# Kernel optimization log

Measured on AMD Instinct MI355X. Metric: run time of the kernel, lower is better.

Reference implementation:

```python
import jax, jax.numpy as jnp
import numpy as np

N_NODES = 50000
N_EDGES = 625000
D = 128


def setup_inputs() -> dict:
    key = jax.random.key(0)
    kx, ks, kr, kw, kb = jax.random.split(key, 5)
    x = jax.random.normal(kx, (N_NODES, D), dtype=jnp.float32)
    senders = jax.random.randint(ks, (N_EDGES,), 0, N_NODES, dtype=jnp.int64)
    receivers = jax.random.randint(kr, (N_EDGES,), 0, N_NODES, dtype=jnp.int64)
    # nn.Linear(2*D, D): weight [D, 2*D], bias [D]
    lim = 1.0 / np.sqrt(2 * D)
    W = jax.random.uniform(kw, (D, 2 * D), minval=-lim, maxval=lim, dtype=jnp.float32)
    b = jax.random.uniform(kb, (D,), minval=-lim, maxval=lim, dtype=jnp.float32)
    return {"x": x, "senders": senders, "receivers": receivers, "n_nodes": N_NODES, "W": W, "b": b}


def reference(x, senders, receivers, n_nodes, W, b):
    # Add self loops (with_self=True)
    self_idx = jnp.arange(n_nodes, dtype=senders.dtype)
    s = jnp.concatenate([senders, self_idx])   # [E + N]
    r = jnp.concatenate([receivers, self_idx]) # [E + N]

    ones = jnp.ones(r.shape[0], dtype=x.dtype)
    # degree_norm=True branch (note: mirrors the original's naming exactly:
    # 'out_degree' counted over receivers, 'in_degree' over senders)
    out_degree = jax.ops.segment_sum(ones, r, num_segments=n_nodes)  # [N]
    in_degree = jax.ops.segment_sum(ones, s, num_segments=n_nodes)   # [N]
    out_degree_norm = jax.lax.rsqrt(jnp.maximum(out_degree, 1.0))
    in_degree_norm = jax.lax.rsqrt(jnp.maximum(in_degree, 1.0))

    # Gather sender embeddings, scale, scatter-add to receivers
    sender_emb = x[s] * out_degree_norm[s][:, None]  # [E+N, D]
    aggregated = jax.ops.segment_sum(sender_emb, r, num_segments=n_nodes)  # [N, D]

    # edge_count over receivers == out_degree (same scatter), clamped
    edge_count = jnp.maximum(out_degree, 1.0)
    aggregated = aggregated / edge_count[:, None]
    aggregated = aggregated * in_degree_norm[:, None]

    combined = jnp.concatenate([x, aggregated], axis=1)  # [N, 2D]
    return combined @ W.T + b
```

## Files before the change

kernel.cpp:

```cpp
#include <hip/hip_runtime.h>

#define DIM 128
#define BM 128
#define BK 32
#define BINSZ 128
#define EPB 2048

typedef __attribute__((ext_vector_type(8))) short short8;
typedef __attribute__((ext_vector_type(4))) float f32x4;

__device__ __forceinline__ unsigned short f2bf(float f) {
    unsigned int b = __float_as_uint(f);
    return (unsigned short)((b + 0x7fffu + ((b >> 16) & 1u)) >> 16);
}
__device__ __forceinline__ float bf_lo(unsigned int u) { return __uint_as_float(u << 16); }
__device__ __forceinline__ float bf_hi(unsigned int u) { return __uint_as_float(u & 0xffff0000u); }
__device__ __forceinline__ unsigned int pack2(float a, float b) {
    return (unsigned int)f2bf(a) | ((unsigned int)f2bf(b) << 16);
}
__device__ __forceinline__ uint2 pack4(float4 v) {
    uint2 r; r.x = pack2(v.x, v.y); r.y = pack2(v.z, v.w); return r;
}

__global__ __launch_bounds__(256) void hist_kernel(
        const int* __restrict__ receivers,
        const float4* __restrict__ W4, uint2* __restrict__ Wb4,
        int* __restrict__ Hr, int* __restrict__ deg_s,
        int E, int nbin, int nw4, int N) {
    __shared__ int hr[512];
    int t = threadIdx.x;

    int gi = blockIdx.x * 256 + t;
    if (gi < nw4) Wb4[gi] = pack4(W4[gi]);
    for (int i = gi; i < N; i += gridDim.x * 256) deg_s[i] = 0;

    for (int b = t; b < nbin; b += 256) hr[b] = 0;
    __syncthreads();
    int base = blockIdx.x * EPB;
    for (int k = 0; k < EPB; k += 256) {
        int e = base + k + t;
        if (e < E) atomicAdd(&hr[receivers[e] >> 7], 1);
    }
    __syncthreads();
    size_t ho = (size_t)blockIdx.x * nbin;
    for (int b = t; b < nbin; b += 256) Hr[ho + b] = hr[b];
}

__global__ __launch_bounds__(512) void scan_bins_kernel(
        int* __restrict__ Hr, int* __restrict__ tot_r, int NAB, int nbin) {
    __shared__ int sr[512];
    int b = blockIdx.x, t = threadIdx.x;
    int vr = (t < NAB) ? Hr[(size_t)t * nbin + b] : 0;
    sr[t] = vr;
    __syncthreads();
    for (int off = 1; off < 512; off <<= 1) {
        int ur = (t >= off) ? sr[t - off] : 0;
        __syncthreads();
        sr[t] += ur;
        __syncthreads();
    }
    if (t < NAB) Hr[(size_t)t * nbin + b] = sr[t] - vr;
    if (t == 511) tot_r[b] = sr[511];
}

__global__ __launch_bounds__(512) void scan_base_kernel(
        const int* __restrict__ tot_r, int* __restrict__ base_r,
        int* __restrict__ row_start, int nbin, int N, int E) {
    __shared__ int sr[512];
    int t = threadIdx.x;
    int vr = (t < nbin) ? tot_r[t] : 0;
    sr[t] = vr;
    __syncthreads();
    for (int off = 1; off < 512; off <<= 1) {
        int ur = (t >= off) ? sr[t - off] : 0;
        __syncthreads();
        sr[t] += ur;
        __syncthreads();
    }
    if (t < nbin) base_r[t] = sr[t] - vr;
    if (t == 0) { base_r[nbin] = E; row_start[N] = E; }
}

__global__ __launch_bounds__(256) void scatter_kernel(
        const int* __restrict__ senders, const int* __restrict__ receivers,
        const int* __restrict__ Hr, const int* __restrict__ base_r,
        unsigned int* __restrict__ bucket_r, int* __restrict__ deg_s,
        int E, int nbin) {
    __shared__ int br_[512];
    int t = threadIdx.x;
    size_t ho = (size_t)blockIdx.x * nbin;
    for (int b = t; b < nbin; b += 256) br_[b] = base_r[b] + Hr[ho + b];
    __syncthreads();
    int base = blockIdx.x * EPB;
    for (int k = 0; k < EPB; k += 256) {
        int e = base + k + t;
        if (e < E) {
            int s = senders[e], r = receivers[e];
            int pr = atomicAdd(&br_[r >> 7], 1);
            bucket_r[pr] = ((unsigned int)(r & 127) << 16) | (unsigned int)s;
            atomicAdd(&deg_s[s], 1);
        }
    }
}

__global__ __launch_bounds__(256) void fine_kernel(
        const unsigned int* __restrict__ bucket_r,
        const int* __restrict__ base_r,
        const int* __restrict__ deg_s,
        const float4* __restrict__ x4,
        uint2* __restrict__ xb2,
        int* __restrict__ edge_src,
        int* __restrict__ row_start,
        float* __restrict__ fs,
        float* __restrict__ sc,
        int N) {
    __shared__ int fine[BINSZ], fstart[BINSZ];
    int b = blockIdx.x, t = threadIdx.x;
    if (t < BINSZ) fine[t] = 0;
    __syncthreads();

    int loR = base_r[b], hiR = base_r[b + 1];
    for (int i = loR + t; i < hiR; i += 256)
        atomicAdd(&fine[bucket_r[i] >> 16], 1);
    __syncthreads();

    if (t < BINSZ) fstart[t] = fine[t];
    __syncthreads();
    for (int off = 1; off < BINSZ; off <<= 1) {
        int u = (t < BINSZ && t >= off) ? fstart[t - off] : 0;
        __syncthreads();
        if (t < BINSZ) fstart[t] += u;
        __syncthreads();
    }
    if (t < BINSZ) {
        int excl = fstart[t] - fine[t];
        int node = b * BINSZ + t;
        if (node < N) {
            float od = (float)(fine[t] + 1);
            row_start[node] = loR + excl;
            sc[node] = rsqrtf(od);
            fs[node] = rsqrtf((float)(deg_s[node] + 1)) / od;
        }
        fstart[t] = excl;
    }
    __syncthreads();

    for (int i = loR + t; i < hiR; i += 256) {
        unsigned int u = bucket_r[i];
        int pos = atomicAdd(&fstart[u >> 16], 1);
        edge_src[loR + pos] = (int)(u & 0xFFFFu);
    }

    int nrow0 = b * BINSZ;
    for (int idx = t; idx < BINSZ * 32; idx += 256) {
        int row = idx >> 5, c = idx & 31;
        int node = nrow0 + row;
        if (node < N) xb2[(size_t)node * 32 + c] = pack4(x4[(size_t)node * 32 + c]);
    }
}

__global__ __launch_bounds__(512) void gemm_kernel(
        const unsigned short* __restrict__ x_bf,
        const int* __restrict__ edge_src,
        const int* __restrict__ row_start,
        const float* __restrict__ fs,
        const float* __restrict__ sc,
        const unsigned short* __restrict__ W_bf,
        const float* __restrict__ bias,
        float* __restrict__ out, int N) {
    __shared__ unsigned short As[BM * BK];
    __shared__ unsigned short Bs[DIM * BK];
    __shared__ unsigned short Agg[BM][136];

    int t    = threadIdx.x;
    int lane = t & 63;
    int w    = t >> 6;
    int wr   = w >> 2, wc = w & 3;
    int row0 = blockIdx.x * BM;
    const uint4* xb4 = (const uint4*)x_bf;

    {
        int grp = lane >> 4;
        int gl  = lane & 15;
        for (int it = 0; it < 4; ++it) {
            int nl = it * 32 + w * 4 + grp;
            int n  = row0 + nl;
            bool valid = (n < N);
            int start = 0, deg = 0;
            if (valid) { start = row_start[n]; deg = row_start[n + 1] - start; }
            int md = deg;
            md = max(md, __shfl_xor(md, 16));
            md = max(md, __shfl_xor(md, 32));

            float a[8];
#pragma unroll
            for (int q = 0; q < 8; q++) a[q] = 0.f;

            for (int base = 0; base < md; base += 16) {
                int e = base + gl;
                int src = -1; float scv = 0.f;
                if (e < deg) { src = edge_src[start + e]; scv = sc[src]; }
#pragma unroll
                for (int j = 0; j < 16; j++) {
                    int   s  = __shfl(src, (grp << 4) | j);
                    float sj = __shfl(scv, (grp << 4) | j);
                    if (s >= 0) {
                        uint4 u = xb4[(size_t)s * 16 + gl];
                        a[0] = fmaf(sj, bf_lo(u.x), a[0]);
                        a[1] = fmaf(sj, bf_hi(u.x), a[1]);
                        a[2] = fmaf(sj, bf_lo(u.y), a[2]);
                        a[3] = fmaf(sj, bf_hi(u.y), a[3]);
                        a[4] = fmaf(sj, bf_lo(u.z), a[4]);
                        a[5] = fmaf(sj, bf_hi(u.z), a[5]);
                        a[6] = fmaf(sj, bf_lo(u.w), a[6]);
                        a[7] = fmaf(sj, bf_hi(u.w), a[7]);
                    }
                }
            }

            uint4 o = make_uint4(0u, 0u, 0u, 0u);
            if (valid) {
                float f = fs[n], scn = sc[n];
                uint4 u = xb4[(size_t)n * 16 + gl];
                a[0] = (a[0] + bf_lo(u.x) * scn) * f;
                a[1] = (a[1] + bf_hi(u.x) * scn) * f;
                a[2] = (a[2] + bf_lo(u.y) * scn) * f;
                a[3] = (a[3] + bf_hi(u.y) * scn) * f;
                a[4] = (a[4] + bf_lo(u.z) * scn) * f;
                a[5] = (a[5] + bf_hi(u.z) * scn) * f;
                a[6] = (a[6] + bf_lo(u.w) * scn) * f;
                a[7] = (a[7] + bf_hi(u.w) * scn) * f;
                o.x = pack2(a[0], a[1]); o.y = pack2(a[2], a[3]);
                o.z = pack2(a[4], a[5]); o.w = pack2(a[6], a[7]);
            }
            *(uint4*)&Agg[nl][gl * 8] = o;
        }
    }
    __syncthreads();

    f32x4 acc[4][2];
#pragma unroll
    for (int i = 0; i < 4; i++)
#pragma unroll
        for (int j = 0; j < 2; j++) acc[i][j] = (f32x4){0.f, 0.f, 0.f, 0.f};

    for (int kt = 0; kt < 8; kt++) {
        int k0 = (kt & 3) * BK;
        if (kt < 4) {
            int row = t >> 2, ch = t & 3;
            uint4 v = *(const uint4*)&x_bf[(size_t)(row0 + row) * 128 + k0 + ch * 8];
            *(uint4*)&As[row * BK + ch * 8] = v;
        }
        {
            int n = t >> 2, ch = t & 3;
            uint4 v = *(const uint4*)&W_bf[(size_t)n * 256 + kt * BK + ch * 8];
            *(uint4*)&Bs[n * BK + ch * 8] = v;
        }
        __syncthreads();

        short8 a[4], b[2];
        if (kt < 4) {
#pragma unroll
            for (int i = 0; i < 4; i++)
                a[i] = *(const short8*)&As[(wr * 64 + i * 16 + (lane & 15)) * BK + (lane >> 4) * 8];
        } else {
#pragma unroll
            for (int i = 0; i < 4; i++)
                a[i] = *(const short8*)&Agg[wr * 64 + i * 16 + (lane & 15)][k0 + (lane >> 4) * 8];
        }
#pragma unroll
        for (int j = 0; j < 2; j++)
            b[j] = *(const short8*)&Bs[(wc * 32 + j * 16 + (lane & 15)) * BK + (lane >> 4) * 8];
#pragma unroll
        for (int i = 0; i < 4; i++)
#pragma unroll
            for (int j = 0; j < 2; j++)
                acc[i][j] = __builtin_amdgcn_mfma_f32_16x16x32_bf16(a[i], b[j], acc[i][j], 0, 0, 0);
        __syncthreads();
    }

    int cq = lane >> 4;
    int cl = lane & 15;
#pragma unroll
    for (int j = 0; j < 2; j++) {
        int col = wc * 32 + j * 16 + cl;
        float bb = bias[col];
#pragma unroll
        for (int i = 0; i < 4; i++) {
            int rbase = row0 + wr * 64 + i * 16 + cq * 4;
#pragma unroll
            for (int r = 0; r < 4; r++) {
                int row = rbase + r;
                if (row < N) out[(size_t)row * DIM + col] = acc[i][j][r] + bb;
            }
        }
    }
}

extern "C" void kernel_launch(void* const* d_in, const int* in_sizes, int n_in,
                              void* d_out, int out_size, void* d_ws, size_t ws_size,
                              hipStream_t stream) {
    const float* x         = (const float*)d_in[0];
    const int*   senders   = (const int*)d_in[1];
    const int*   receivers = (const int*)d_in[2];
    const float* W         = (const float*)d_in[4];
    const float* bias      = (const float*)d_in[5];
    float*       out       = (float*)d_out;

    int N    = in_sizes[0] / DIM;
    int E    = in_sizes[1];
    int nbin = (N + BINSZ - 1) / BINSZ;
    int NAB  = (E + EPB - 1) / EPB;
    int NP   = ((N + BM - 1) / BM) * BM;

    char* ws = (char*)d_ws;
    size_t off = 0;
    #define WS_ALLOC(ptrtype, name, bytes) \
        ptrtype name = (ptrtype)(ws + off); off += (((size_t)(bytes)) + 255) & ~(size_t)255;
    WS_ALLOC(int*,            tot_r,     (size_t)nbin * 4)
    WS_ALLOC(int*,            base_r,    (size_t)(nbin + 1) * 4)
    WS_ALLOC(int*,            row_start, (size_t)(N + 1) * 4)
    WS_ALLOC(float*,          fs,        (size_t)N * 4)
    WS_ALLOC(float*,          sc,        (size_t)N * 4)
    WS_ALLOC(int*,            deg_s,     (size_t)N * 4)
    WS_ALLOC(int*,            edge_src,  (size_t)E * 4)
    WS_ALLOC(unsigned short*, x_bf,      (size_t)NP * DIM * 2)
    WS_ALLOC(unsigned short*, W_bf,      (size_t)DIM * 256 * 2)
    WS_ALLOC(unsigned int*,   bucket_r,  (size_t)E * 4)
    WS_ALLOC(int*,            Hr,        (size_t)NAB * nbin * 4)
    #undef WS_ALLOC

    int nw4 = DIM * 256 / 4;

    hist_kernel<<<NAB, 256, 0, stream>>>(receivers,
                                         (const float4*)W, (uint2*)W_bf,
                                         Hr, deg_s, E, nbin, nw4, N);
    scan_bins_kernel<<<nbin, 512, 0, stream>>>(Hr, tot_r, NAB, nbin);
    scan_base_kernel<<<1, 512, 0, stream>>>(tot_r, base_r, row_start, nbin, N, E);
    scatter_kernel<<<NAB, 256, 0, stream>>>(senders, receivers, Hr, base_r,
                                            bucket_r, deg_s, E, nbin);
    fine_kernel<<<nbin, 256, 0, stream>>>(bucket_r, base_r, deg_s,
                                          (const float4*)x, (uint2*)x_bf,
                                          edge_src, row_start, fs, sc, N);
    gemm_kernel<<<(N + BM - 1) / BM, 512, 0, stream>>>(
        x_bf, edge_src, row_start, fs, sc, W_bf, bias, out, N);
}
```

Baseline: 196.3 us.

## Split neighbor gather into its own kernel and pack source index with bf16 scale

Moves the per-node neighbor aggregation out of the GEMM kernel into a separate gather kernel with one 16-lane group per node across many small blocks. The result goes to a bf16 buffer in global memory that the GEMM then streams through shared memory like x. The sender index and its bf16-rounded scale are packed into one 32-bit word, so each edge needs one shuffle instead of two. This aims to improve occupancy and load balance of the latency-bound gather, at the cost of an extra launch, a global round trip for the aggregate, and rounding the scale to bf16.

```diff
diff --git a/kernel.cpp b/kernel.cpp
--- a/kernel.cpp
+++ b/kernel.cpp
@@ -138,7 +138,7 @@
         if (node < N) {
             float od = (float)(fine[t] + 1);
             row_start[node] = loR + excl;
-            sc[node] = rsqrtf(od);
+            sc[node] = __uint_as_float((unsigned int)f2bf(rsqrtf(od)) << 16);
             fs[node] = rsqrtf((float)(deg_s[node] + 1)) / od;
         }
         fstart[t] = excl;
@@ -159,84 +159,89 @@
     }
 }
 
-__global__ __launch_bounds__(512) void gemm_kernel(
-        const unsigned short* __restrict__ x_bf,
+__global__ __launch_bounds__(256) void gather_kernel(
+        const uint4* __restrict__ xb4,
         const int* __restrict__ edge_src,
         const int* __restrict__ row_start,
         const float* __restrict__ fs,
         const float* __restrict__ sc,
+        uint4* __restrict__ aggb4,
+        int N) {
+    int lane = threadIdx.x & 63;
+    int grp  = lane >> 4;
+    int gl   = lane & 15;
+    int wid  = (blockIdx.x * blockDim.x + threadIdx.x) >> 6;
+    int n    = wid * 4 + grp;
+    bool valid = (n < N);
+
+    int start = 0, deg = 0;
+    if (valid) { start = row_start[n]; deg = row_start[n + 1] - start; }
+    int md = deg;
+    md = max(md, __shfl_xor(md, 16));
+    md = max(md, __shfl_xor(md, 32));
+
+    float a[8];
+#pragma unroll
+    for (int q = 0; q < 8; q++) a[q] = 0.f;
+
+    for (int base = 0; base < md; base += 16) {
+        int e = base + gl;
+        unsigned int pk = 0xFFFFFFFFu;
+        if (e < deg) {
+            int s = edge_src[start + e];
+            pk = (unsigned int)s | (__float_as_uint(sc[s]) & 0xffff0000u);
+        }
+#pragma unroll
+        for (int j = 0; j < 16; j++) {
+            unsigned int u = (unsigned int)__shfl((int)pk, (grp << 4) | j);
+            if (u != 0xFFFFFFFFu) {
+                int   s  = (int)(u & 0xFFFFu);
+                float sj = bf_hi(u);
+                uint4 v  = xb4[(size_t)s * 16 + gl];
+                a[0] = fmaf(sj, bf_lo(v.x), a[0]);
+                a[1] = fmaf(sj, bf_hi(v.x), a[1]);
+                a[2] = fmaf(sj, bf_lo(v.y), a[2]);
+                a[3] = fmaf(sj, bf_hi(v.y), a[3]);
+                a[4] = fmaf(sj, bf_lo(v.z), a[4]);
+                a[5] = fmaf(sj, bf_hi(v.z), a[5]);
+                a[6] = fmaf(sj, bf_lo(v.w), a[6]);
+                a[7] = fmaf(sj, bf_hi(v.w), a[7]);
+            }
+        }
+    }
+
+    if (valid) {
+        float f = fs[n], scn = sc[n];
+        uint4 u = xb4[(size_t)n * 16 + gl];
+        a[0] = (a[0] + bf_lo(u.x) * scn) * f;
+        a[1] = (a[1] + bf_hi(u.x) * scn) * f;
+        a[2] = (a[2] + bf_lo(u.y) * scn) * f;
+        a[3] = (a[3] + bf_hi(u.y) * scn) * f;
+        a[4] = (a[4] + bf_lo(u.z) * scn) * f;
+        a[5] = (a[5] + bf_hi(u.z) * scn) * f;
+        a[6] = (a[6] + bf_lo(u.w) * scn) * f;
+        a[7] = (a[7] + bf_hi(u.w) * scn) * f;
+        uint4 o;
+        o.x = pack2(a[0], a[1]); o.y = pack2(a[2], a[3]);
+        o.z = pack2(a[4], a[5]); o.w = pack2(a[6], a[7]);
+        aggb4[(size_t)n * 16 + gl] = o;
+    }
+}
+
+__global__ __launch_bounds__(512) void gemm_kernel(
+        const unsigned short* __restrict__ x_bf,
+        const unsigned short* __restrict__ agg_bf,
         const unsigned short* __restrict__ W_bf,
         const float* __restrict__ bias,
         float* __restrict__ out, int N) {
     __shared__ unsigned short As[BM * BK];
     __shared__ unsigned short Bs[DIM * BK];
-    __shared__ unsigned short Agg[BM][136];
 
     int t    = threadIdx.x;
     int lane = t & 63;
     int w    = t >> 6;
     int wr   = w >> 2, wc = w & 3;
     int row0 = blockIdx.x * BM;
-    const uint4* xb4 = (const uint4*)x_bf;
-
-    {
-        int grp = lane >> 4;
-        int gl  = lane & 15;
-        for (int it = 0; it < 4; ++it) {
-            int nl = it * 32 + w * 4 + grp;
-            int n  = row0 + nl;
-            bool valid = (n < N);
-            int start = 0, deg = 0;
-            if (valid) { start = row_start[n]; deg = row_start[n + 1] - start; }
-            int md = deg;
-            md = max(md, __shfl_xor(md, 16));
-            md = max(md, __shfl_xor(md, 32));
-
-            float a[8];
-#pragma unroll
-            for (int q = 0; q < 8; q++) a[q] = 0.f;
-
-            for (int base = 0; base < md; base += 16) {
-                int e = base + gl;
-                int src = -1; float scv = 0.f;
-                if (e < deg) { src = edge_src[start + e]; scv = sc[src]; }
-#pragma unroll
-                for (int j = 0; j < 16; j++) {
-                    int   s  = __shfl(src, (grp << 4) | j);
-                    float sj = __shfl(scv, (grp << 4) | j);
-                    if (s >= 0) {
-                        uint4 u = xb4[(size_t)s * 16 + gl];
-                        a[0] = fmaf(sj, bf_lo(u.x), a[0]);
-                        a[1] = fmaf(sj, bf_hi(u.x), a[1]);
-                        a[2] = fmaf(sj, bf_lo(u.y), a[2]);
-                        a[3] = fmaf(sj, bf_hi(u.y), a[3]);
-                        a[4] = fmaf(sj, bf_lo(u.z), a[4]);
-                        a[5] = fmaf(sj, bf_hi(u.z), a[5]);
-                        a[6] = fmaf(sj, bf_lo(u.w), a[6]);
-                        a[7] = fmaf(sj, bf_hi(u.w), a[7]);
-                    }
-                }
-            }
-
-            uint4 o = make_uint4(0u, 0u, 0u, 0u);
-            if (valid) {
-                float f = fs[n], scn = sc[n];
-                uint4 u = xb4[(size_t)n * 16 + gl];
-                a[0] = (a[0] + bf_lo(u.x) * scn) * f;
-                a[1] = (a[1] + bf_hi(u.x) * scn) * f;
-                a[2] = (a[2] + bf_lo(u.y) * scn) * f;
-                a[3] = (a[3] + bf_hi(u.y) * scn) * f;
-                a[4] = (a[4] + bf_lo(u.z) * scn) * f;
-                a[5] = (a[5] + bf_hi(u.z) * scn) * f;
-                a[6] = (a[6] + bf_lo(u.w) * scn) * f;
-                a[7] = (a[7] + bf_hi(u.w) * scn) * f;
-                o.x = pack2(a[0], a[1]); o.y = pack2(a[2], a[3]);
-                o.z = pack2(a[4], a[5]); o.w = pack2(a[6], a[7]);
-            }
-            *(uint4*)&Agg[nl][gl * 8] = o;
-        }
-    }
-    __syncthreads();
 
     f32x4 acc[4][2];
 #pragma unroll
@@ -245,10 +250,11 @@
         for (int j = 0; j < 2; j++) acc[i][j] = (f32x4){0.f, 0.f, 0.f, 0.f};
 
     for (int kt = 0; kt < 8; kt++) {
+        const unsigned short* src = (kt < 4) ? x_bf : agg_bf;
         int k0 = (kt & 3) * BK;
-        if (kt < 4) {
+        {
             int row = t >> 2, ch = t & 3;
-            uint4 v = *(const uint4*)&x_bf[(size_t)(row0 + row) * 128 + k0 + ch * 8];
+            uint4 v = *(const uint4*)&src[(size_t)(row0 + row) * 128 + k0 + ch * 8];
             *(uint4*)&As[row * BK + ch * 8] = v;
         }
         {
@@ -259,15 +265,9 @@
         __syncthreads();
 
         short8 a[4], b[2];
-        if (kt < 4) {
-#pragma unroll
-            for (int i = 0; i < 4; i++)
-                a[i] = *(const short8*)&As[(wr * 64 + i * 16 + (lane & 15)) * BK + (lane >> 4) * 8];
-        } else {
-#pragma unroll
-            for (int i = 0; i < 4; i++)
-                a[i] = *(const short8*)&Agg[wr * 64 + i * 16 + (lane & 15)][k0 + (lane >> 4) * 8];
-        }
+#pragma unroll
+        for (int i = 0; i < 4; i++)
+            a[i] = *(const short8*)&As[(wr * 64 + i * 16 + (lane & 15)) * BK + (lane >> 4) * 8];
 #pragma unroll
         for (int j = 0; j < 2; j++)
             b[j] = *(const short8*)&Bs[(wc * 32 + j * 16 + (lane & 15)) * BK + (lane >> 4) * 8];
@@ -325,6 +325,7 @@
     WS_ALLOC(int*,            deg_s,     (size_t)N * 4)
     WS_ALLOC(int*,            edge_src,  (size_t)E * 4)
     WS_ALLOC(unsigned short*, x_bf,      (size_t)NP * DIM * 2)
+    WS_ALLOC(unsigned short*, agg_bf,    (size_t)NP * DIM * 2)
     WS_ALLOC(unsigned short*, W_bf,      (size_t)DIM * 256 * 2)
     WS_ALLOC(unsigned int*,   bucket_r,  (size_t)E * 4)
     WS_ALLOC(int*,            Hr,        (size_t)NAB * nbin * 4)
@@ -342,6 +343,10 @@
     fine_kernel<<<nbin, 256, 0, stream>>>(bucket_r, base_r, deg_s,
                                           (const float4*)x, (uint2*)x_bf,
                                           edge_src, row_start, fs, sc, N);
+    int nwave = (N + 3) / 4;
+    gather_kernel<<<(nwave * 64 + 255) / 256, 256, 0, stream>>>(
+        (const uint4*)x_bf, edge_src, row_start, fs, sc,
+        (uint4*)agg_bf, N);
     gemm_kernel<<<(N + BM - 1) / BM, 512, 0, stream>>>(
-        x_bf, edge_src, row_start, fs, sc, W_bf, bias, out, N);
-}
+        x_bf, agg_bf, W_bf, bias, out, N);
+}
```

Measured after the change: 190.8 us. -2.8%, faster.
